# Optimization experiments

Measured on AMD Instinct MI355X. Metric: run time of the kernel, lower is better.

The kernel has to match this reference:

```python
import jax, jax.numpy as jnp
import numpy as np
from functools import partial

EPS = 1e-6
SINKHORN_ITERS = 10

def sinkhorn(logits):
    # log-space Sinkhorn normalization -> doubly-stochastic soft permutation
    M = logits
    for _ in range(SINKHORN_ITERS):
        M = M - jax.scipy.special.logsumexp(M, axis=1, keepdims=True)
        M = M - jax.scipy.special.logsumexp(M, axis=0, keepdims=True)
    return jnp.exp(M)

def r_poly(a):
    delta = 0.5 - a
    num = 0.25 + 1.65811 * delta + 2.15388 * delta**2 + 8.2844 * delta**3 + 6.16764 * delta**4
    den = a * (1.0 - a)
    den = jnp.where(jnp.abs(den) < EPS, EPS, den)
    return num / den

def power_r(x, y, ra, w0, w1):
    ra = jnp.where(jnp.abs(ra) < EPS, EPS, ra)
    return (w0 * x**ra + w1 * y**ra) ** (1.0 / ra)

def F_upper(x, y, a, w0, w1):
    # generalized combine for a in [0.5, 2); x,y pre-clamped to [EPS, 1-EPS]
    xy = x * y
    mn = jnp.minimum(x, y)
    lin = w0 * x + w1 * y
    p = jnp.sqrt(jnp.maximum(3.0 / jnp.maximum(2.0 - a, EPS) - 1.0, EPS))
    r1 = xy ** p                                      # 1.25 < a < 2
    r3 = 4.0 * ((1.25 - a) * mn + (a - 1.0) * xy)     # 1 < a < 1.25
    ra = r_poly(jnp.clip(a, 0.75, 1.0 - EPS))
    r5 = power_r(x, y, ra, w0, w1)                    # 0.75 <= a < 1
    R = r_poly(jnp.float32(0.75))
    r6 = (3.0 - 4.0 * a) * lin + (4.0 * a - 2.0) * power_r(x, y, R, w0, w1)
    r0 = jnp.where((jnp.abs(x - 1.0) < EPS) & (jnp.abs(y - 1.0) < EPS), 1.0, 0.0)
    out = lin                                          # a ~ 0.5 / fallback
    out = jnp.where((a > 0.5) & (a < 0.75), r6, out)
    out = jnp.where((a >= 0.75) & (a < 1.0), r5, out)
    out = jnp.where(jnp.abs(a - 1.0) < EPS, mn, out)
    out = jnp.where((a > 1.0) & (a < 1.25), r3, out)
    out = jnp.where(jnp.abs(a - 1.25) < EPS, xy, out)
    out = jnp.where((a > 1.25) & (a < 2.0), r1, out)
    out = jnp.where(jnp.abs(a - 2.0) < EPS, r0, out)
    return out

def F_comb(x, y, a, w0, w1):
    x = jnp.clip(jnp.nan_to_num(x, nan=EPS), EPS, 1.0 - EPS)
    y = jnp.clip(jnp.nan_to_num(y, nan=EPS), EPS, 1.0 - EPS)
    a = jnp.clip(jnp.nan_to_num(a, nan=-1.0, posinf=2.0 - EPS, neginf=-1.0 + EPS), -1.0 + EPS, 2.0 - EPS)
    hi = F_upper(x, y, a, w0, w1)
    a_flip = jnp.clip(1.0 - a, -1.0 + EPS, 2.0 - EPS)
    lo = 1.0 - F_upper(1.0 - x, 1.0 - y, a_flip, w0, w1)  # rule 8 (single-level recursion)
    return jnp.where(a < 0.5 - EPS, lo, hi)

def combine(left, right, w, b):
    w_soft = jax.nn.softmax(w)
    a_scaled = jax.nn.sigmoid(b) * 3.0 - 1.0
    nres = F_comb(left, right, a_scaled, w_soft[0], w_soft[1])
    return jnp.where(jnp.isnan(nres), a_scaled, nres)

def setup_inputs() -> dict:
    key = jax.random.key(0)
    k1, k2, k3, k4 = jax.random.split(key, 4)
    B, L = 65536, 256
    x = jax.random.uniform(k1, (B, L), dtype=jnp.float32)
    logits = jax.random.normal(k2, (L, L), dtype=jnp.float32)
    weights = jax.random.uniform(k3, (L - 1, 2), dtype=jnp.float32) + 0.5   # uniform(0.5, 1.5)
    biases = jax.random.uniform(k4, (L - 1,), dtype=jnp.float32) * 3.0 - 1.0
    return {"x": x, "logits": logits, "weights": weights, "biases": biases}

def reference(x, logits, weights, biases):
    P = sinkhorn(logits)                  # (L, L) soft permutation
    leaf_values = x @ P                   # (B, L)
    leaves = leaf_values.T                # (L, B)
    out0 = combine(leaves[0], leaves[1], weights[0], biases[0])

    def step(carry, inp):
        leaf, w, b = inp
        out = combine(carry, leaf, w, b)
        return out, None

    final, _ = jax.lax.scan(step, out0, (leaves[2:], weights[1:], biases[1:]))
    return final[:, None]                 # (B, 1)
```

## Files before the change

kernel.cpp:

```cpp
#include <hip/hip_runtime.h>

#define EPS 1e-6f

typedef unsigned short u16;
typedef u16   u16x4  __attribute__((ext_vector_type(4)));
typedef u16   u16x8  __attribute__((ext_vector_type(8)));
typedef float f32x4  __attribute__((ext_vector_type(4)));
typedef _Float16 f16x8 __attribute__((ext_vector_type(8)));

enum { BR_LIN = 0, BR_R6, BR_R5, BR_MIN, BR_R3, BR_XY, BR_R1, BR_R0 };

__device__ __forceinline__ u16 f2h(float f) { return __builtin_bit_cast(u16, (_Float16)f); }

__device__ __forceinline__ f16x8 lds_f16x8(const u16* p) {
  u16x8 r = *(const u16x8*)p;
  return __builtin_bit_cast(f16x8, r);
}

__device__ __forceinline__ f32x4 mfma16(f16x8 a, f16x8 b, f32x4 c) {
  return __builtin_amdgcn_mfma_f32_16x16x32_f16(a, b, c, 0, 0, 0);
}

__device__ __forceinline__ float fexp2(float x) {
  float r; asm("v_exp_f32 %0, %1" : "=v"(r) : "v"(x)); return r;
}
__device__ __forceinline__ float flog2(float x) {
  float r; asm("v_log_f32 %0, %1" : "=v"(r) : "v"(x)); return r;
}

__device__ __forceinline__ float r_poly_f(float a) {
  float d  = 0.5f - a;
  float d2 = d * d;
  float num = 0.25f + 1.65811f * d + 2.15388f * d2 + 8.2844f * d2 * d + 6.16764f * d2 * d2;
  float den = a * (1.0f - a);
  if (fabsf(den) < EPS) den = EPS;
  return num / den;
}

__device__ __forceinline__ void leaf_pre(float leaf, f32x4 p0, f32x4 p2,
                                         float& Y, float& w1Y, float& w1ey, float& cply) {
  float fx = p0[0], w1 = p0[2], rs = p2[0], cp = p2[2], sx = p2[3];
  float yy = fminf(fmaxf(leaf, EPS), 1.0f - EPS);
  Y = fmaf(sx, yy, fx);
  float ly = flog2(Y);
  w1Y  = w1 * Y;
  w1ey = w1 * fexp2(rs * ly);
  cply = cp * ly;
}

__device__ __forceinline__ float step_carry(float carry, float Y, float w1Y, float w1ey, float cply,
                                            f32x4 p0, f32x4 p1, f32x4 p2) {
  float fx = p0[0], w0 = p0[1], s_lin = p0[3];
  float s_mn = p1[0], s_xy = p1[1], s_pm = p1[2], s_pow = p1[3];
  float rs = p2[0], rinv = p2[1], cp = p2[2], sx = p2[3];

  float xx = fminf(fmaxf(carry, EPS), 1.0f - EPS);
  float X  = fmaf(sx, xx, fx);
  float lx = flog2(X);
  float pw = fexp2(fmaf(cp, lx, cply));
  float ex = fexp2(rs * lx);
  float s  = fmaf(w0, ex, w1ey);
  float pm = fexp2(rinv * flog2(s));

  float r = s_lin * fmaf(w0, X, w1Y);
  r = fmaf(s_mn, fminf(X, Y), r);
  r = fmaf(s_xy, X * Y, r);
  r = fmaf(s_pm, pm, r);
  r = fmaf(s_pow, pw, r);
  return fmaf(sx, r, fx);
}

__global__ void param_kernel(const float* __restrict__ W, const float* __restrict__ Bv,
                             float* __restrict__ prm12, int n) {
  int i = blockIdx.x * blockDim.x + threadIdx.x;
  if (i >= n) return;
  float w0r = W[2 * i], w1r = W[2 * i + 1];
  float m  = fmaxf(w0r, w1r);
  float e0 = expf(w0r - m), e1 = expf(w1r - m);
  float inv = 1.0f / (e0 + e1);
  float w0 = e0 * inv, w1 = e1 * inv;

  float b   = Bv[i];
  float sig = 1.0f / (1.0f + expf(-b));
  float a_fb = sig * 3.0f - 1.0f;

  float a = a_fb;
  if (__builtin_isnan(a)) a = -1.0f;
  a = fminf(fmaxf(a, -1.0f + EPS), 2.0f - EPS);
  int flip = (a < 0.5f - EPS) ? 1 : 0;
  float aa = a;
  if (flip) aa = fminf(fmaxf(1.0f - a, -1.0f + EPS), 2.0f - EPS);

  int br; float c0 = 0.f, c1 = 0.f, c2 = 0.f, c3 = 0.f;
  if (fabsf(aa - 2.0f) < EPS) br = BR_R0;
  else if (aa > 1.25f && aa < 2.0f) {
    br = BR_R1;
    c0 = sqrtf(fmaxf(3.0f / fmaxf(2.0f - aa, EPS) - 1.0f, EPS));
  } else if (fabsf(aa - 1.25f) < EPS) br = BR_XY;
  else if (aa > 1.0f && aa < 1.25f) { br = BR_R3; c0 = 1.25f - aa; c1 = aa - 1.0f; }
  else if (fabsf(aa - 1.0f) < EPS) br = BR_MIN;
  else if (aa >= 0.75f && aa < 1.0f) {
    br = BR_R5;
    float ac = fminf(fmaxf(aa, 0.75f), 1.0f - EPS);
    float ra = r_poly_f(ac);
    if (fabsf(ra) < EPS) ra = EPS;
    c0 = ra; c1 = 1.0f / ra;
  } else if (aa > 0.5f && aa < 0.75f) {
    br = BR_R6;
    c0 = 3.0f - 4.0f * aa; c1 = 4.0f * aa - 2.0f;
    float R = r_poly_f(0.75f);
    if (fabsf(R) < EPS) R = EPS;
    c2 = R; c3 = 1.0f / R;
  } else br = BR_LIN;

  float s_lin = 0.f, s_mn = 0.f, s_xy = 0.f, s_pm = 0.f, s_pow = 0.f;
  float rs = 1.0f, rinv = 1.0f, cp = 0.0f;
  if (br == BR_R1)       { s_pow = 1.0f; cp = c0; }
  else if (br == BR_XY)  { s_xy = 1.0f; }
  else if (br == BR_R3)  { s_mn = 4.0f * c0; s_xy = 4.0f * c1; }
  else if (br == BR_MIN) { s_mn = 1.0f; }
  else if (br == BR_R5)  { s_pm = 1.0f; rs = c0; rinv = c1; }
  else if (br == BR_R6)  { s_lin = c0; s_pm = c1; rs = c2; rinv = c3; }
  else if (br == BR_LIN) { s_lin = 1.0f; }

  float* o12 = prm12 + i * 12;
  o12[0] = (float)flip; o12[1] = w0;  o12[2] = w1;   o12[3] = s_lin;
  o12[4] = s_mn;        o12[5] = s_xy; o12[6] = s_pm; o12[7] = s_pow;
  o12[8] = rs;          o12[9] = rinv; o12[10] = cp;  o12[11] = 1.0f - 2.0f * (float)flip;
}

__global__ __launch_bounds__(1024, 4) void sinkhorn_kernel(
    const float* __restrict__ logits, u16* __restrict__ PTf) {
  __shared__ float alpha[256], beta[256];
  __shared__ float psum[256][33];

  const int t  = threadIdx.x;
  const int R  = t >> 5;
  const int C  = t & 31;
  const int r0 = R << 3;

  float e[8][8];
  #pragma unroll
  for (int dr = 0; dr < 8; ++dr) {
    const float* row = logits + (r0 + dr) * 256 + C;
    #pragma unroll
    for (int m = 0; m < 8; ++m) e[dr][m] = __expf(row[m << 5]);
  }

  if (t < 256) beta[t] = 1.0f;
  __syncthreads();

  for (int it = 0; it < 10; ++it) {
    {
      float bv[8], acc[8];
      #pragma unroll
      for (int m = 0; m < 8; ++m) bv[m] = beta[C + (m << 5)];
      #pragma unroll
      for (int dr = 0; dr < 8; ++dr) {
        float s = 0.f;
        #pragma unroll
        for (int m = 0; m < 8; ++m) s += e[dr][m] * bv[m];
        acc[dr] = s;
      }
      #pragma unroll
      for (int dr = 0; dr < 8; ++dr) psum[r0 + dr][C] = acc[dr];
    }
    __syncthreads();
    if (t < 256) {
      float s = 0.f;
      #pragma unroll
      for (int j = 0; j < 32; ++j) s += psum[t][j];
      alpha[t] = 1.0f / s;
    }
    __syncthreads();
    {
      float av[8], acc[8];
      #pragma unroll
      for (int dr = 0; dr < 8; ++dr) av[dr] = alpha[r0 + dr];
      #pragma unroll
      for (int m = 0; m < 8; ++m) {
        float s = 0.f;
        #pragma unroll
        for (int dr = 0; dr < 8; ++dr) s += e[dr][m] * av[dr];
        acc[m] = s;
      }
      #pragma unroll
      for (int m = 0; m < 8; ++m) psum[C + (m << 5)][R] = acc[m];
    }
    __syncthreads();
    if (t < 256) {
      float s = 0.f;
      #pragma unroll
      for (int j = 0; j < 32; ++j) s += psum[t][j];
      beta[t] = 1.0f / s;
    }
    __syncthreads();
  }

  float av[8], bv[8];
  #pragma unroll
  for (int dr = 0; dr < 8; ++dr) av[dr] = alpha[r0 + dr];
  #pragma unroll
  for (int m = 0; m < 8; ++m) bv[m] = beta[C + (m << 5)];

  #pragma unroll
  for (int m = 0; m < 8; ++m) {
    int l = C + (m << 5);
    u16x8 vh;
    #pragma unroll
    for (int dr = 0; dr < 8; ++dr) vh[dr] = f2h(av[dr] * e[dr][m] * bv[m]);
    *(u16x8*)(PTf + l * 256 + r0) = vh;
  }
}

#define CSTR 132

__global__ __launch_bounds__(512, 4) void gemm_chain_kernel(
    const float* __restrict__ x, const u16* __restrict__ PTf,
    const float* __restrict__ prm12, float* __restrict__ out) {
  __shared__ __align__(16) char smem[46080];
  u16* xs = (u16*)smem;
  u16* pt = (u16*)(smem + 8192);
  float* cbuf = (float*)smem;
  float* qlds = (float*)(smem + 33792);

  const int t    = threadIdx.x;
  const int w    = t >> 6;
  const int lane = t & 63;
  const int bl   = lane & 15;
  const int kh   = lane >> 4;
  const int wm   = w >> 2;
  const int wn   = w & 3;
  const int b0   = blockIdx.x * 128;

  const int xrow = t >> 3;
  const int xc4  = t & 7;

  for (int j = t; j < 3060; j += 512) qlds[j] = prm12[j];

  f32x4 acc[8][2];
  #pragma unroll
  for (int m = 0; m < 8; ++m) {
    acc[m][0] = f32x4{0.f, 0.f, 0.f, 0.f};
    acc[m][1] = f32x4{0.f, 0.f, 0.f, 0.f};
  }

  f32x4 xr[2];
  u16x8 pr[2];

  #pragma unroll
  for (int j = 0; j < 2; ++j) {
    xr[j] = *(const f32x4*)(x + (b0 + xrow + 64 * j) * 256 + (xc4 << 2));
    int c = t + 512 * j, r = c >> 2, s = c & 3, g = s ^ ((r >> 1) & 3);
    pr[j] = *(const u16x8*)(PTf + r * 256 + (g << 3));
  }

  for (int kc = 0; kc < 8; ++kc) {
    #pragma unroll
    for (int j = 0; j < 2; ++j) {
      int row = xrow + 64 * j;
      u16x4 hv;
      #pragma unroll
      for (int e = 0; e < 4; ++e) hv[e] = f2h(xr[j][e]);
      int g = xc4 >> 1, sub = xc4 & 1;
      *(u16x4*)(xs + row * 32 + ((g ^ ((row >> 1) & 3)) << 3) + (sub << 2)) = hv;
      *(u16x8*)(pt + ((t + 512 * j) << 3)) = pr[j];
    }
    __syncthreads();

    if (kc < 7) {
      int k1 = (kc + 1) << 5;
      #pragma unroll
      for (int j = 0; j < 2; ++j) {
        xr[j] = *(const f32x4*)(x + (b0 + xrow + 64 * j) * 256 + k1 + (xc4 << 2));
        int c = t + 512 * j, r = c >> 2, s = c & 3, g = s ^ ((r >> 1) & 3);
        pr[j] = *(const u16x8*)(PTf + r * 256 + k1 + (g << 3));
      }
    }

    f16x8 bh[2];
    #pragma unroll
    for (int nf = 0; nf < 2; ++nf) {
      int brow = (wn << 5) + (nf << 4) + bl;
      bh[nf] = lds_f16x8(xs + brow * 32 + ((kh ^ ((brow >> 1) & 3)) << 3));
    }
    #pragma unroll
    for (int mf = 0; mf < 8; ++mf) {
      int arow = (wm << 7) + (mf << 4) + bl;
      f16x8 ah = lds_f16x8(pt + arow * 32 + ((kh ^ ((arow >> 1) & 3)) << 3));
      #pragma unroll
      for (int nf = 0; nf < 2; ++nf)
        acc[mf][nf] = mfma16(ah, bh[nf], acc[mf][nf]);
    }
    __syncthreads();
  }

  float carry = 0.0f;

  #pragma unroll
  for (int c = 0; c < 4; ++c) {
    __syncthreads();
    if (wm == (c >> 1)) {
      #pragma unroll
      for (int d = 0; d < 4; ++d) {
        int mf = ((c & 1) << 2) + d;
        #pragma unroll
        for (int nf = 0; nf < 2; ++nf) {
          int bc = (wn << 5) + (nf << 4) + bl;
          #pragma unroll
          for (int r = 0; r < 4; ++r) {
            int lr = (d << 4) + (kh << 2) + r;
            cbuf[lr * CSTR + bc] = acc[mf][nf][r];
          }
        }
      }
    }
    __syncthreads();
    if (t < 128) {
      int lc0 = 0;
      if (c == 0) {
        float v0 = cbuf[0 * CSTR + t];
        float v1 = cbuf[1 * CSTR + t];
        float v2 = cbuf[2 * CSTR + t];
        float v3 = cbuf[3 * CSTR + t];
        carry = v0;
        float vv[3] = {v1, v2, v3};
        #pragma unroll
        for (int u = 0; u < 3; ++u) {
          const float* qn = qlds + u * 12;
          f32x4 P0 = *(const f32x4*)(qn), P1 = *(const f32x4*)(qn + 4), P2 = *(const f32x4*)(qn + 8);
          float Y, w1Y, w1ey, cply;
          leaf_pre(vv[u], P0, P2, Y, w1Y, w1ey, cply);
          carry = step_carry(carry, Y, w1Y, w1ey, cply, P0, P1, P2);
        }
        lc0 = 4;
      }
      for (int lc = lc0; lc < 64; lc += 4) {
        float v[4];
        #pragma unroll
        for (int u = 0; u < 4; ++u) v[u] = cbuf[(lc + u) * CSTR + t];
        f32x4 P0[4], P1[4], P2[4];
        #pragma unroll
        for (int u = 0; u < 4; ++u) {
          const float* qn = qlds + ((c << 6) + lc + u - 1) * 12;
          P0[u] = *(const f32x4*)(qn);
          P1[u] = *(const f32x4*)(qn + 4);
          P2[u] = *(const f32x4*)(qn + 8);
        }
        float Y[4], w1Y[4], w1ey[4], cply[4];
        #pragma unroll
        for (int u = 0; u < 4; ++u)
          leaf_pre(v[u], P0[u], P2[u], Y[u], w1Y[u], w1ey[u], cply[u]);
        #pragma unroll
        for (int u = 0; u < 4; ++u)
          carry = step_carry(carry, Y[u], w1Y[u], w1ey[u], cply[u], P0[u], P1[u], P2[u]);
      }
    }
  }
  if (t < 128) out[b0 + t] = carry;
}

extern "C" void kernel_launch(void* const* d_in, const int* in_sizes, int n_in,
                              void* d_out, int out_size, void* d_ws, size_t ws_size,
                              hipStream_t stream) {
  const float* x       = (const float*)d_in[0];
  const float* logits  = (const float*)d_in[1];
  const float* weights = (const float*)d_in[2];
  const float* biases  = (const float*)d_in[3];
  float* out = (float*)d_out;

  char* ws = (char*)d_ws;
  int Btot = in_sizes[0] / 256;

  u16*   PTf   = (u16*)ws;
  float* prm12 = (float*)(ws + 131072);

  param_kernel<<<1, 256, 0, stream>>>(weights, biases, prm12, 255);
  sinkhorn_kernel<<<1, 1024, 0, stream>>>(logits, PTf);
  gemm_chain_kernel<<<Btot / 128, 512, 0, stream>>>(x, PTf, prm12, out);
}
```

Before: 81.14 us.

## Fold param kernel into sinkhorn and halve gemm-chain block to 64 rows

Moves the per-node parameter computation into the sinkhorn kernel, removing one kernel launch. Shrinks the GEMM+chain block from 128 batch rows and 512 threads to 64 rows and 256 threads, doubling the grid to 1024 blocks and cutting LDS per block. The goal is better CU occupancy and shorter serial chain tails per block. In exchange each block reloads the full P tile for fewer rows, so P traffic per output doubles and the prm12 copy into LDS is repeated across twice as many blocks.

```diff
diff --git a/kernel.cpp b/kernel.cpp
--- a/kernel.cpp
+++ b/kernel.cpp
@@ -70,71 +70,72 @@
   return fmaf(sx, r, fx);
 }
 
-__global__ void param_kernel(const float* __restrict__ W, const float* __restrict__ Bv,
-                             float* __restrict__ prm12, int n) {
-  int i = blockIdx.x * blockDim.x + threadIdx.x;
-  if (i >= n) return;
-  float w0r = W[2 * i], w1r = W[2 * i + 1];
-  float m  = fmaxf(w0r, w1r);
-  float e0 = expf(w0r - m), e1 = expf(w1r - m);
-  float inv = 1.0f / (e0 + e1);
-  float w0 = e0 * inv, w1 = e1 * inv;
-
-  float b   = Bv[i];
-  float sig = 1.0f / (1.0f + expf(-b));
-  float a_fb = sig * 3.0f - 1.0f;
-
-  float a = a_fb;
-  if (__builtin_isnan(a)) a = -1.0f;
-  a = fminf(fmaxf(a, -1.0f + EPS), 2.0f - EPS);
-  int flip = (a < 0.5f - EPS) ? 1 : 0;
-  float aa = a;
-  if (flip) aa = fminf(fmaxf(1.0f - a, -1.0f + EPS), 2.0f - EPS);
-
-  int br; float c0 = 0.f, c1 = 0.f, c2 = 0.f, c3 = 0.f;
-  if (fabsf(aa - 2.0f) < EPS) br = BR_R0;
-  else if (aa > 1.25f && aa < 2.0f) {
-    br = BR_R1;
-    c0 = sqrtf(fmaxf(3.0f / fmaxf(2.0f - aa, EPS) - 1.0f, EPS));
-  } else if (fabsf(aa - 1.25f) < EPS) br = BR_XY;
-  else if (aa > 1.0f && aa < 1.25f) { br = BR_R3; c0 = 1.25f - aa; c1 = aa - 1.0f; }
-  else if (fabsf(aa - 1.0f) < EPS) br = BR_MIN;
-  else if (aa >= 0.75f && aa < 1.0f) {
-    br = BR_R5;
-    float ac = fminf(fmaxf(aa, 0.75f), 1.0f - EPS);
-    float ra = r_poly_f(ac);
-    if (fabsf(ra) < EPS) ra = EPS;
-    c0 = ra; c1 = 1.0f / ra;
-  } else if (aa > 0.5f && aa < 0.75f) {
-    br = BR_R6;
-    c0 = 3.0f - 4.0f * aa; c1 = 4.0f * aa - 2.0f;
-    float R = r_poly_f(0.75f);
-    if (fabsf(R) < EPS) R = EPS;
-    c2 = R; c3 = 1.0f / R;
-  } else br = BR_LIN;
-
-  float s_lin = 0.f, s_mn = 0.f, s_xy = 0.f, s_pm = 0.f, s_pow = 0.f;
-  float rs = 1.0f, rinv = 1.0f, cp = 0.0f;
-  if (br == BR_R1)       { s_pow = 1.0f; cp = c0; }
-  else if (br == BR_XY)  { s_xy = 1.0f; }
-  else if (br == BR_R3)  { s_mn = 4.0f * c0; s_xy = 4.0f * c1; }
-  else if (br == BR_MIN) { s_mn = 1.0f; }
-  else if (br == BR_R5)  { s_pm = 1.0f; rs = c0; rinv = c1; }
-  else if (br == BR_R6)  { s_lin = c0; s_pm = c1; rs = c2; rinv = c3; }
-  else if (br == BR_LIN) { s_lin = 1.0f; }
-
-  float* o12 = prm12 + i * 12;
-  o12[0] = (float)flip; o12[1] = w0;  o12[2] = w1;   o12[3] = s_lin;
-  o12[4] = s_mn;        o12[5] = s_xy; o12[6] = s_pm; o12[7] = s_pow;
-  o12[8] = rs;          o12[9] = rinv; o12[10] = cp;  o12[11] = 1.0f - 2.0f * (float)flip;
-}
-
 __global__ __launch_bounds__(1024, 4) void sinkhorn_kernel(
-    const float* __restrict__ logits, u16* __restrict__ PTf) {
+    const float* __restrict__ logits, u16* __restrict__ PTf,
+    const float* __restrict__ W, const float* __restrict__ Bv,
+    float* __restrict__ prm12) {
+  const int t  = threadIdx.x;
+
+  if (t < 255) {
+    int i = t;
+    float w0r = W[2 * i], w1r = W[2 * i + 1];
+    float m  = fmaxf(w0r, w1r);
+    float e0 = expf(w0r - m), e1 = expf(w1r - m);
+    float inv = 1.0f / (e0 + e1);
+    float w0 = e0 * inv, w1 = e1 * inv;
+
+    float b   = Bv[i];
+    float sig = 1.0f / (1.0f + expf(-b));
+    float a_fb = sig * 3.0f - 1.0f;
+
+    float a = a_fb;
+    if (__builtin_isnan(a)) a = -1.0f;
+    a = fminf(fmaxf(a, -1.0f + EPS), 2.0f - EPS);
+    int flip = (a < 0.5f - EPS) ? 1 : 0;
+    float aa = a;
+    if (flip) aa = fminf(fmaxf(1.0f - a, -1.0f + EPS), 2.0f - EPS);
+
+    int br; float c0 = 0.f, c1 = 0.f, c2 = 0.f, c3 = 0.f;
+    if (fabsf(aa - 2.0f) < EPS) br = BR_R0;
+    else if (aa > 1.25f && aa < 2.0f) {
+      br = BR_R1;
+      c0 = sqrtf(fmaxf(3.0f / fmaxf(2.0f - aa, EPS) - 1.0f, EPS));
+    } else if (fabsf(aa - 1.25f) < EPS) br = BR_XY;
+    else if (aa > 1.0f && aa < 1.25f) { br = BR_R3; c0 = 1.25f - aa; c1 = aa - 1.0f; }
+    else if (fabsf(aa - 1.0f) < EPS) br = BR_MIN;
+    else if (aa >= 0.75f && aa < 1.0f) {
+      br = BR_R5;
+      float ac = fminf(fmaxf(aa, 0.75f), 1.0f - EPS);
+      float ra = r_poly_f(ac);
+      if (fabsf(ra) < EPS) ra = EPS;
+      c0 = ra; c1 = 1.0f / ra;
+    } else if (aa > 0.5f && aa < 0.75f) {
+      br = BR_R6;
+      c0 = 3.0f - 4.0f * aa; c1 = 4.0f * aa - 2.0f;
+      float R = r_poly_f(0.75f);
+      if (fabsf(R) < EPS) R = EPS;
+      c2 = R; c3 = 1.0f / R;
+    } else br = BR_LIN;
+
+    float s_lin = 0.f, s_mn = 0.f, s_xy = 0.f, s_pm = 0.f, s_pow = 0.f;
+    float rs = 1.0f, rinv = 1.0f, cp = 0.0f;
+    if (br == BR_R1)       { s_pow = 1.0f; cp = c0; }
+    else if (br == BR_XY)  { s_xy = 1.0f; }
+    else if (br == BR_R3)  { s_mn = 4.0f * c0; s_xy = 4.0f * c1; }
+    else if (br == BR_MIN) { s_mn = 1.0f; }
+    else if (br == BR_R5)  { s_pm = 1.0f; rs = c0; rinv = c1; }
+    else if (br == BR_R6)  { s_lin = c0; s_pm = c1; rs = c2; rinv = c3; }
+    else if (br == BR_LIN) { s_lin = 1.0f; }
+
+    float* o12 = prm12 + i * 12;
+    o12[0] = (float)flip; o12[1] = w0;  o12[2] = w1;   o12[3] = s_lin;
+    o12[4] = s_mn;        o12[5] = s_xy; o12[6] = s_pm; o12[7] = s_pow;
+    o12[8] = rs;          o12[9] = rinv; o12[10] = cp;  o12[11] = 1.0f - 2.0f * (float)flip;
+  }
+
   __shared__ float alpha[256], beta[256];
   __shared__ float psum[256][33];
 
-  const int t  = threadIdx.x;
   const int R  = t >> 5;
   const int C  = t & 31;
   const int r0 = R << 3;
@@ -213,30 +214,30 @@
   }
 }
 
-#define CSTR 132
-
-__global__ __launch_bounds__(512, 4) void gemm_chain_kernel(
+#define CSTR 68
+
+__global__ __launch_bounds__(256, 4) void gemm_chain_kernel(
     const float* __restrict__ x, const u16* __restrict__ PTf,
     const float* __restrict__ prm12, float* __restrict__ out) {
-  __shared__ __align__(16) char smem[46080];
+  __shared__ __align__(16) char smem[32768];
   u16* xs = (u16*)smem;
-  u16* pt = (u16*)(smem + 8192);
+  u16* pt = (u16*)(smem + 4096);
+  float* qlds = (float*)(smem + 20480);
   float* cbuf = (float*)smem;
-  float* qlds = (float*)(smem + 33792);
 
   const int t    = threadIdx.x;
   const int w    = t >> 6;
   const int lane = t & 63;
   const int bl   = lane & 15;
   const int kh   = lane >> 4;
-  const int wm   = w >> 2;
-  const int wn   = w & 3;
-  const int b0   = blockIdx.x * 128;
-
-  const int xrow = t >> 3;
-  const int xc4  = t & 7;
-
-  for (int j = t; j < 3060; j += 512) qlds[j] = prm12[j];
+  const int wm   = w >> 1;
+  const int wn   = w & 1;
+  const int b0   = blockIdx.x * 64;
+
+  const int xrow = t >> 2;
+  const int xsl  = t & 3;
+
+  for (int j = t; j < 3060; j += 256) qlds[j] = prm12[j];
 
   f32x4 acc[8][2];
   #pragma unroll
@@ -246,34 +247,40 @@
   }
 
   f32x4 xr[2];
-  u16x8 pr[2];
-
-  #pragma unroll
-  for (int j = 0; j < 2; ++j) {
-    xr[j] = *(const f32x4*)(x + (b0 + xrow + 64 * j) * 256 + (xc4 << 2));
-    int c = t + 512 * j, r = c >> 2, s = c & 3, g = s ^ ((r >> 1) & 3);
+  u16x8 pr[4];
+
+  #pragma unroll
+  for (int j = 0; j < 2; ++j)
+    xr[j] = *(const f32x4*)(x + (b0 + xrow) * 256 + ((xsl + 4 * j) << 2));
+  #pragma unroll
+  for (int j = 0; j < 4; ++j) {
+    int c = t + 256 * j, r = c >> 2, s = c & 3, g = s ^ ((r >> 1) & 3);
     pr[j] = *(const u16x8*)(PTf + r * 256 + (g << 3));
   }
 
   for (int kc = 0; kc < 8; ++kc) {
     #pragma unroll
     for (int j = 0; j < 2; ++j) {
-      int row = xrow + 64 * j;
+      int slot = xsl + 4 * j;
       u16x4 hv;
       #pragma unroll
       for (int e = 0; e < 4; ++e) hv[e] = f2h(xr[j][e]);
-      int g = xc4 >> 1, sub = xc4 & 1;
-      *(u16x4*)(xs + row * 32 + ((g ^ ((row >> 1) & 3)) << 3) + (sub << 2)) = hv;
-      *(u16x8*)(pt + ((t + 512 * j) << 3)) = pr[j];
-    }
+      int g = slot >> 1, sub = slot & 1;
+      *(u16x4*)(xs + xrow * 32 + ((g ^ ((xrow >> 1) & 3)) << 3) + (sub << 2)) = hv;
+    }
+    #pragma unroll
+    for (int j = 0; j < 4; ++j)
+      *(u16x8*)(pt + ((t + 256 * j) << 3)) = pr[j];
     __syncthreads();
 
     if (kc < 7) {
       int k1 = (kc + 1) << 5;
       #pragma unroll
-      for (int j = 0; j < 2; ++j) {
-        xr[j] = *(const f32x4*)(x + (b0 + xrow + 64 * j) * 256 + k1 + (xc4 << 2));
-        int c = t + 512 * j, r = c >> 2, s = c & 3, g = s ^ ((r >> 1) & 3);
+      for (int j = 0; j < 2; ++j)
+        xr[j] = *(const f32x4*)(x + (b0 + xrow) * 256 + k1 + ((xsl + 4 * j) << 2));
+      #pragma unroll
+      for (int j = 0; j < 4; ++j) {
+        int c = t + 256 * j, r = c >> 2, s = c & 3, g = s ^ ((r >> 1) & 3);
         pr[j] = *(const u16x8*)(PTf + r * 256 + k1 + (g << 3));
       }
     }
@@ -316,7 +323,7 @@
       }
     }
     __syncthreads();
-    if (t < 128) {
+    if (t < 64) {
       int lc0 = 0;
       if (c == 0) {
         float v0 = cbuf[0 * CSTR + t];
@@ -357,7 +364,7 @@
       }
     }
   }
-  if (t < 128) out[b0 + t] = carry;
+  if (t < 64) out[b0 + t] = carry;
 }
 
 extern "C" void kernel_launch(void* const* d_in, const int* in_sizes, int n_in,
@@ -375,7 +382,6 @@
   u16*   PTf   = (u16*)ws;
   float* prm12 = (float*)(ws + 131072);
 
-  param_kernel<<<1, 256, 0, stream>>>(weights, biases, prm12, 255);
-  sinkhorn_kernel<<<1, 1024, 0, stream>>>(logits, PTf);
-  gemm_chain_kernel<<<Btot / 128, 512, 0, stream>>>(x, PTf, prm12, out);
-}
+  sinkhorn_kernel<<<1, 1024, 0, stream>>>(logits, PTf, weights, biases, prm12);
+  gemm_chain_kernel<<<Btot / 64, 256, 0, stream>>>(x, PTf, prm12, out);
+}
```

After: 70.26 us. 1.15x faster.
